# Performance work log

Measured on AMD Instinct MI355X. Metric: run time of the kernel, lower is better.

The kernel has to match this reference:

```python
import jax, jax.numpy as jnp
import numpy as np

B, S, H, D = 8, 16, 32, 64
HID = H * D
PAST = 4096


def setup_inputs() -> dict:
    key = jax.random.key(0)
    ks = jax.random.split(key, 7)
    sc = 0.02
    return {
        "hidden_states": jax.random.normal(ks[0], (B, S, HID), jnp.float32),
        "past_k": jax.random.normal(ks[1], (B, H, PAST, D), jnp.float32),
        "past_v": jax.random.normal(ks[2], (B, H, PAST, D), jnp.float32),
        "wq": jax.random.normal(ks[3], (HID, HID), jnp.float32) * sc,
        "wk": jax.random.normal(ks[4], (HID, HID), jnp.float32) * sc,
        "wv": jax.random.normal(ks[5], (HID, HID), jnp.float32) * sc,
        "wo": jax.random.normal(ks[6], (HID, HID), jnp.float32) * sc,
    }


def reference(hidden_states, past_k, past_v, wq, wk, wv, wo):
    b, s, _ = hidden_states.shape
    # QKV projections (torch Linear: x @ W.T), split into heads -> [B,H,S,D]
    q = (hidden_states @ wq.T).reshape(b, s, H, D).transpose(0, 2, 1, 3)
    k = (hidden_states @ wk.T).reshape(b, s, H, D).transpose(0, 2, 1, 3)
    v = (hidden_states @ wv.T).reshape(b, s, H, D).transpose(0, 2, 1, 3)
    # KV-cache concat: [B,H,past+S,D]
    k = jnp.concatenate([past_k, k], axis=2)
    v = jnp.concatenate([past_v, v], axis=2)
    scale = 1.0 / jnp.sqrt(jnp.asarray(D, hidden_states.dtype))
    # scores [B,H,S,T]
    scores = jnp.einsum("bhsd,bhtd->bhst", q, k) * scale
    probs = jax.nn.softmax(scores, axis=-1)
    out = jnp.einsum("bhst,bhtd->bhsd", probs, v)
    out = out.transpose(0, 2, 1, 3).reshape(b, s, HID)
    return out @ wo.T
```

## Files before the change

### kernel.cpp

```cpp
#include <hip/hip_runtime.h>
#include <hip/hip_bf16.h>
#include <stdint.h>

#define HID 2048
#define NH  32
#define HD  64
#define NB  8
#define NS  16
#define PAST 4096

#define QSCALE 0.18033688011112042591f

typedef __attribute__((ext_vector_type(8))) short short8;
typedef __attribute__((ext_vector_type(4))) short short4v;
typedef __attribute__((ext_vector_type(4))) float f32x4;

#define MFMA(a, b, c) __builtin_amdgcn_mfma_f32_16x16x32_bf16((a), (b), (c), 0, 0, 0)

#define PART_STRIDE 1088
#define NSPLIT 4

static __device__ __forceinline__ short f2bf(float f) {
    __hip_bfloat16 h = __float2bfloat16(f);
    return *reinterpret_cast<short*>(&h);
}

static __device__ __forceinline__ short8 pack8(float4 a, float4 b) {
    short8 r;
    r[0] = f2bf(a.x); r[1] = f2bf(a.y); r[2] = f2bf(a.z); r[3] = f2bf(a.w);
    r[4] = f2bf(b.x); r[5] = f2bf(b.y); r[6] = f2bf(b.z); r[7] = f2bf(b.w);
    return r;
}

static __device__ __forceinline__ short8 pack8s(float4 a, float4 b, float s) {
    short8 r;
    r[0] = f2bf(a.x * s); r[1] = f2bf(a.y * s); r[2] = f2bf(a.z * s); r[3] = f2bf(a.w * s);
    r[4] = f2bf(b.x * s); r[5] = f2bf(b.y * s); r[6] = f2bf(b.z * s); r[7] = f2bf(b.w * s);
    return r;
}

__global__ __launch_bounds__(256) void cvt_kernel(const float* __restrict__ in,
                                                  short* __restrict__ out) {
    int i = (blockIdx.x * 256 + threadIdx.x) * 4;
    float4 v = *reinterpret_cast<const float4*>(in + i);
    short4v o;
    o[0] = f2bf(v.x); o[1] = f2bf(v.y); o[2] = f2bf(v.z); o[3] = f2bf(v.w);
    *reinterpret_cast<short4v*>(out + i) = o;
}

__global__ __launch_bounds__(128) void proj_kernel(
        const short* __restrict__ X,
        const float* __restrict__ W0, const float* __restrict__ W1,
        const float* __restrict__ W2,
        float* __restrict__ Y0, float* __restrict__ Y1, float* __restrict__ Y2) {
    int mat   = blockIdx.x >> 9;
    int rest  = blockIdx.x & 511;
    int strip = rest >> 2, ks = rest & 3;
    int nbase = strip * 16;
    int k0    = ks * 512;
    const float* W = (mat == 0) ? W0 : (mat == 1) ? W1 : W2;
    float*       Y = (mat == 0) ? Y0 : (mat == 1) ? Y1 : Y2;

    int lane = threadIdx.x & 63;
    int wave = threadIdx.x >> 6;
    int lr = lane & 15, g = lane >> 4;

    f32x4 acc0 = {0.f, 0.f, 0.f, 0.f};
    f32x4 acc1 = {0.f, 0.f, 0.f, 0.f};
    f32x4 acc2 = {0.f, 0.f, 0.f, 0.f};
    f32x4 acc3 = {0.f, 0.f, 0.f, 0.f};

    const short* xr = X + (size_t)(wave * 64 + lr) * HID + g * 8 + k0;
    const float* wr = W + (size_t)(nbase + lr) * HID + g * 8 + k0;

    #pragma unroll 4
    for (int kc = 0; kc < 512; kc += 32) {
        float4 w0 = *reinterpret_cast<const float4*>(wr + kc);
        float4 w1 = *reinterpret_cast<const float4*>(wr + kc + 4);
        short8 bb = pack8(w0, w1);
        short8 a0 = *reinterpret_cast<const short8*>(xr + kc);
        short8 a1 = *reinterpret_cast<const short8*>(xr + (size_t)16 * HID + kc);
        short8 a2 = *reinterpret_cast<const short8*>(xr + (size_t)32 * HID + kc);
        short8 a3 = *reinterpret_cast<const short8*>(xr + (size_t)48 * HID + kc);
        acc0 = MFMA(a0, bb, acc0);
        acc1 = MFMA(a1, bb, acc1);
        acc2 = MFMA(a2, bb, acc2);
        acc3 = MFMA(a3, bb, acc3);
    }
    #define STACC(accv, f) do { \
        atomicAdd(&Y[(size_t)(wave * 64 + (f) * 16 + (g << 2) + 0) * HID + nbase + lr], accv[0]); \
        atomicAdd(&Y[(size_t)(wave * 64 + (f) * 16 + (g << 2) + 1) * HID + nbase + lr], accv[1]); \
        atomicAdd(&Y[(size_t)(wave * 64 + (f) * 16 + (g << 2) + 2) * HID + nbase + lr], accv[2]); \
        atomicAdd(&Y[(size_t)(wave * 64 + (f) * 16 + (g << 2) + 3) * HID + nbase + lr], accv[3]); \
    } while (0)
    STACC(acc0, 0); STACC(acc1, 1); STACC(acc2, 2); STACC(acc3, 3);
    #undef STACC
}

__global__ __launch_bounds__(256, 4) void attn_kernel(
        const float* __restrict__ q,
        const float* __restrict__ knew, const float* __restrict__ vnew,
        const float* __restrict__ pastK, const float* __restrict__ pastV,
        float* __restrict__ parts) {
    int bid = blockIdx.x;
    int bh = bid >> 2, split = bid & 3;
    int b = bh >> 5, h = bh & 31;
    int wave = threadIdx.x >> 6, lane = threadIdx.x & 63;
    int lq = lane & 15, g = lane >> 4;

    const float* qp = q + (size_t)(b * NS + lq) * HID + h * HD + g * 8;
    short8 qf0, qf1;
    {
        float4 a0 = *reinterpret_cast<const float4*>(qp);
        float4 a1 = *reinterpret_cast<const float4*>(qp + 4);
        float4 a2 = *reinterpret_cast<const float4*>(qp + 32);
        float4 a3 = *reinterpret_cast<const float4*>(qp + 36);
        qf0 = pack8s(a0, a1, QSCALE);
        qf1 = pack8s(a2, a3, QSCALE);
    }

    f32x4 o0 = {0.f, 0.f, 0.f, 0.f};
    f32x4 o1 = {0.f, 0.f, 0.f, 0.f};
    f32x4 o2 = {0.f, 0.f, 0.f, 0.f};
    f32x4 o3 = {0.f, 0.f, 0.f, 0.f};
    float m = -__builtin_inff(), lsum = 0.0f;

    const float* kbase = pastK + (size_t)bh * PAST * HD + (size_t)(split * 1024 + wave * 256) * HD;
    const float* vbase = pastV + (size_t)bh * PAST * HD + (size_t)(split * 1024 + wave * 256) * HD;

    #define LOADV8(dst, vtp, kfo, dcol) do { \
        dst[0] = f2bf((vtp)[(size_t)((kfo) + (g << 2) + 0) * HD + (dcol)]); \
        dst[1] = f2bf((vtp)[(size_t)((kfo) + (g << 2) + 1) * HD + (dcol)]); \
        dst[2] = f2bf((vtp)[(size_t)((kfo) + (g << 2) + 2) * HD + (dcol)]); \
        dst[3] = f2bf((vtp)[(size_t)((kfo) + (g << 2) + 3) * HD + (dcol)]); \
        dst[4] = f2bf((vtp)[(size_t)((kfo) + 16 + (g << 2) + 0) * HD + (dcol)]); \
        dst[5] = f2bf((vtp)[(size_t)((kfo) + 16 + (g << 2) + 1) * HD + (dcol)]); \
        dst[6] = f2bf((vtp)[(size_t)((kfo) + 16 + (g << 2) + 2) * HD + (dcol)]); \
        dst[7] = f2bf((vtp)[(size_t)((kfo) + 16 + (g << 2) + 3) * HD + (dcol)]); \
    } while (0)

    #define QKSUB(scv, s2i) do { \
        const float* kr = kbase + (size_t)(pb + (s2i) * 16 + lq) * HD + (g << 3); \
        float4 ka = *reinterpret_cast<const float4*>(kr); \
        float4 kb2 = *reinterpret_cast<const float4*>(kr + 4); \
        float4 kc2 = *reinterpret_cast<const float4*>(kr + 32); \
        float4 kd2 = *reinterpret_cast<const float4*>(kr + 36); \
        short8 af0 = pack8(ka, kb2); \
        short8 af1 = pack8(kc2, kd2); \
        f32x4 sv = {0.f, 0.f, 0.f, 0.f}; \
        sv = MFMA(af0, qf0, sv); \
        sv = MFMA(af1, qf1, sv); \
        scv = sv; \
    } while (0)

    #define PEXP(dst, idx, sv, r) do { \
        float e = exp2f(sv[r] - mn); rsum += e; dst[idx] = f2bf(e); \
    } while (0)

    #pragma unroll 1
    for (int t = 0; t < 4; ++t) {
        int pb = t * 64;

        const float* vt = vbase + (size_t)pb * HD;
        short8 vf0, vf1, vf2, vf3, vf4, vf5, vf6, vf7;
        LOADV8(vf0, vt, 0,  lq);       LOADV8(vf1, vt, 32, lq);
        LOADV8(vf2, vt, 0,  16 + lq);  LOADV8(vf3, vt, 32, 16 + lq);
        LOADV8(vf4, vt, 0,  32 + lq);  LOADV8(vf5, vt, 32, 32 + lq);
        LOADV8(vf6, vt, 0,  48 + lq);  LOADV8(vf7, vt, 32, 48 + lq);

        f32x4 sc0, sc1, sc2, sc3;
        QKSUB(sc0, 0); QKSUB(sc1, 1); QKSUB(sc2, 2); QKSUB(sc3, 3);

        float tmax = fmaxf(
            fmaxf(fmaxf(fmaxf(sc0[0], sc0[1]), fmaxf(sc0[2], sc0[3])),
                  fmaxf(fmaxf(sc1[0], sc1[1]), fmaxf(sc1[2], sc1[3]))),
            fmaxf(fmaxf(fmaxf(sc2[0], sc2[1]), fmaxf(sc2[2], sc2[3])),
                  fmaxf(fmaxf(sc3[0], sc3[1]), fmaxf(sc3[2], sc3[3]))));
        tmax = fmaxf(tmax, __shfl_xor(tmax, 16));
        tmax = fmaxf(tmax, __shfl_xor(tmax, 32));
        float mn = fmaxf(m, tmax);
        float alpha = exp2f(m - mn);
        float rsum = 0.f;
        short8 pf0, pf1;
        PEXP(pf0, 0, sc0, 0); PEXP(pf0, 1, sc0, 1); PEXP(pf0, 2, sc0, 2); PEXP(pf0, 3, sc0, 3);
        PEXP(pf0, 4, sc1, 0); PEXP(pf0, 5, sc1, 1); PEXP(pf0, 6, sc1, 2); PEXP(pf0, 7, sc1, 3);
        PEXP(pf1, 0, sc2, 0); PEXP(pf1, 1, sc2, 1); PEXP(pf1, 2, sc2, 2); PEXP(pf1, 3, sc2, 3);
        PEXP(pf1, 4, sc3, 0); PEXP(pf1, 5, sc3, 1); PEXP(pf1, 6, sc3, 2); PEXP(pf1, 7, sc3, 3);
        rsum += __shfl_xor(rsum, 16);
        rsum += __shfl_xor(rsum, 32);
        lsum = lsum * alpha + rsum;
        m = mn;
        o0 *= alpha; o1 *= alpha; o2 *= alpha; o3 *= alpha;

        o0 = MFMA(vf0, pf0, o0); o0 = MFMA(vf1, pf1, o0);
        o1 = MFMA(vf2, pf0, o1); o1 = MFMA(vf3, pf1, o1);
        o2 = MFMA(vf4, pf0, o2); o2 = MFMA(vf5, pf1, o2);
        o3 = MFMA(vf6, pf0, o3); o3 = MFMA(vf7, pf1, o3);
    }

    if (split == 0 && wave == 0) {
        const float* kr = knew + (size_t)(b * NS + lq) * HID + h * HD + g * 8;
        float4 ka = *reinterpret_cast<const float4*>(kr);
        float4 kb2 = *reinterpret_cast<const float4*>(kr + 4);
        float4 kc2 = *reinterpret_cast<const float4*>(kr + 32);
        float4 kd2 = *reinterpret_cast<const float4*>(kr + 36);
        short8 af0 = pack8(ka, kb2);
        short8 af1 = pack8(kc2, kd2);
        f32x4 sv = {0.f, 0.f, 0.f, 0.f};
        sv = MFMA(af0, qf0, sv);
        sv = MFMA(af1, qf1, sv);

        float tmax = fmaxf(fmaxf(sv[0], sv[1]), fmaxf(sv[2], sv[3]));
        tmax = fmaxf(tmax, __shfl_xor(tmax, 16));
        tmax = fmaxf(tmax, __shfl_xor(tmax, 32));
        float mn = fmaxf(m, tmax);
        float alpha = exp2f(m - mn);
        float e0 = exp2f(sv[0] - mn);
        float e1 = exp2f(sv[1] - mn);
        float e2 = exp2f(sv[2] - mn);
        float e3 = exp2f(sv[3] - mn);
        float rsum = e0 + e1 + e2 + e3;
        rsum += __shfl_xor(rsum, 16);
        rsum += __shfl_xor(rsum, 32);
        lsum = lsum * alpha + rsum;
        m = mn;
        o0 *= alpha; o1 *= alpha; o2 *= alpha; o3 *= alpha;

        short8 pfT;
        pfT[0] = f2bf(e0); pfT[1] = f2bf(e1); pfT[2] = f2bf(e2); pfT[3] = f2bf(e3);
        pfT[4] = 0; pfT[5] = 0; pfT[6] = 0; pfT[7] = 0;

        const float* vt = vnew + (size_t)(b * NS) * HID + h * HD;
        #define LOADVT(dst, dcol) do { \
            dst[0] = f2bf(vt[(size_t)((g << 2) + 0) * HID + (dcol)]); \
            dst[1] = f2bf(vt[(size_t)((g << 2) + 1) * HID + (dcol)]); \
            dst[2] = f2bf(vt[(size_t)((g << 2) + 2) * HID + (dcol)]); \
            dst[3] = f2bf(vt[(size_t)((g << 2) + 3) * HID + (dcol)]); \
            dst[4] = 0; dst[5] = 0; dst[6] = 0; dst[7] = 0; \
        } while (0)
        short8 vv0, vv1, vv2, vv3;
        LOADVT(vv0, lq); LOADVT(vv1, 16 + lq); LOADVT(vv2, 32 + lq); LOADVT(vv3, 48 + lq);
        #undef LOADVT
        o0 = MFMA(vv0, pfT, o0);
        o1 = MFMA(vv1, pfT, o1);
        o2 = MFMA(vv2, pfT, o2);
        o3 = MFMA(vv3, pfT, o3);
    }

    __shared__ float s_o[4][16][64];
    __shared__ float s_m[4][16];
    __shared__ float s_l[4][16];
    #define STO(ov, dt) do { \
        s_o[wave][lq][(dt) * 16 + (g << 2) + 0] = ov[0]; \
        s_o[wave][lq][(dt) * 16 + (g << 2) + 1] = ov[1]; \
        s_o[wave][lq][(dt) * 16 + (g << 2) + 2] = ov[2]; \
        s_o[wave][lq][(dt) * 16 + (g << 2) + 3] = ov[3]; \
    } while (0)
    STO(o0, 0); STO(o1, 1); STO(o2, 2); STO(o3, 3);
    #undef STO
    if (g == 0) { s_m[wave][lq] = m; s_l[wave][lq] = lsum; }
    __syncthreads();

    if (wave == 0) {
        float M = fmaxf(fmaxf(s_m[0][lq], s_m[1][lq]), fmaxf(s_m[2][lq], s_m[3][lq]));
        float aw0 = exp2f(s_m[0][lq] - M);
        float aw1 = exp2f(s_m[1][lq] - M);
        float aw2 = exp2f(s_m[2][lq] - M);
        float aw3 = exp2f(s_m[3][lq] - M);
        float L = aw0 * s_l[0][lq] + aw1 * s_l[1][lq] + aw2 * s_l[2][lq] + aw3 * s_l[3][lq];
        float* pbase = parts + (size_t)bid * PART_STRIDE;
        if (g == 0) { pbase[lq] = M; pbase[16 + lq] = L; }
        for (int dd = 0; dd < 16; ++dd) {
            int di = g * 16 + dd;
            float v = aw0 * s_o[0][lq][di] + aw1 * s_o[1][lq][di] +
                      aw2 * s_o[2][lq][di] + aw3 * s_o[3][lq][di];
            pbase[32 + lq * 64 + di] = v;
        }
    }
}

__global__ __launch_bounds__(256) void merge_kernel(const float* __restrict__ parts,
                                                    short* __restrict__ attnb) {
    int bh = blockIdx.x;
    int tid = threadIdx.x;
    int qi = tid >> 4, ds = (tid & 15) * 4;
    const float* p0 = parts + (size_t)(bh * NSPLIT) * PART_STRIDE;
    const float* p1 = p0 + PART_STRIDE;
    const float* p2 = p1 + PART_STRIDE;
    const float* p3 = p2 + PART_STRIDE;
    float m0 = p0[qi], m1 = p1[qi], m2 = p2[qi], m3 = p3[qi];
    float M = fmaxf(fmaxf(m0, m1), fmaxf(m2, m3));
    float a0 = exp2f(m0 - M), a1 = exp2f(m1 - M), a2 = exp2f(m2 - M), a3 = exp2f(m3 - M);
    float inv = 1.0f / (a0 * p0[16 + qi] + a1 * p1[16 + qi] +
                        a2 * p2[16 + qi] + a3 * p3[16 + qi]);
    int b = bh >> 5, h = bh & 31;
    int base = 32 + qi * 64 + ds;
    float v0 = (a0 * p0[base + 0] + a1 * p1[base + 0] + a2 * p2[base + 0] + a3 * p3[base + 0]) * inv;
    float v1 = (a0 * p0[base + 1] + a1 * p1[base + 1] + a2 * p2[base + 1] + a3 * p3[base + 1]) * inv;
    float v2 = (a0 * p0[base + 2] + a1 * p1[base + 2] + a2 * p2[base + 2] + a3 * p3[base + 2]) * inv;
    float v3 = (a0 * p0[base + 3] + a1 * p1[base + 3] + a2 * p2[base + 3] + a3 * p3[base + 3]) * inv;
    short4v o;
    o[0] = f2bf(v0); o[1] = f2bf(v1); o[2] = f2bf(v2); o[3] = f2bf(v3);
    *reinterpret_cast<short4v*>(attnb + (size_t)(b * NS + qi) * HID + h * HD + ds) = o;
}

extern "C" void kernel_launch(void* const* d_in, const int* in_sizes, int n_in,
                              void* d_out, int out_size, void* d_ws, size_t ws_size,
                              hipStream_t stream) {
    const float* hs     = (const float*)d_in[0];
    const float* past_k = (const float*)d_in[1];
    const float* past_v = (const float*)d_in[2];
    const float* wq     = (const float*)d_in[3];
    const float* wk     = (const float*)d_in[4];
    const float* wv     = (const float*)d_in[5];
    const float* wo     = (const float*)d_in[6];
    float* out = (float*)d_out;

    float* qb = (float*)d_ws;
    float* kn = qb + 128 * 2048;
    float* vn = kn + 128 * 2048;
    short* hsb   = (short*)(vn + 128 * 2048);
    short* attnb = hsb + 128 * 2048;
    float* parts = (float*)(attnb + 128 * 2048);

    hipMemsetAsync(qb, 0, (size_t)3 * 128 * 2048 * sizeof(float), stream);
    hipMemsetAsync(out, 0, (size_t)128 * 2048 * sizeof(float), stream);

    cvt_kernel<<<256, 256, 0, stream>>>(hs, hsb);
    proj_kernel<<<1536, 128, 0, stream>>>(hsb, wq, wk, wv, qb, kn, vn);
    attn_kernel<<<256 * NSPLIT, 256, 0, stream>>>(qb, kn, vn, past_k, past_v, parts);
    merge_kernel<<<256, 256, 0, stream>>>(parts, attnb);
    proj_kernel<<<512, 128, 0, stream>>>(attnb, wo, wo, wo, out, out, out);
}
```

Measured before the change: 179.6 us.

## Stage V tiles through per-wave LDS with coalesced loads and hoisted K loads

Previously each lane gathered V elements with strided scalar global loads to form the transposed MFMA operand. Now each wave loads V rows with coalesced float4 loads, converts them to bf16 into a padded per-wave LDS slab, and reads the transposed fragments back from LDS. K loads for all four subtiles are hoisted before the MFMAs to increase memory-level parallelism. The LDS slab is reused for the final cross-wave reduction behind an extra barrier, which adds LDS traffic and register pressure in exchange for fewer uncoalesced global accesses.

```diff
diff --git a/kernel.cpp b/kernel.cpp
--- a/kernel.cpp
+++ b/kernel.cpp
@@ -19,6 +19,7 @@
 
 #define PART_STRIDE 1088
 #define NSPLIT 4
+#define VSLAB  8704
 
 static __device__ __forceinline__ short f2bf(float f) {
     __hip_bfloat16 h = __float2bfloat16(f);
@@ -29,6 +30,12 @@
     short8 r;
     r[0] = f2bf(a.x); r[1] = f2bf(a.y); r[2] = f2bf(a.z); r[3] = f2bf(a.w);
     r[4] = f2bf(b.x); r[5] = f2bf(b.y); r[6] = f2bf(b.z); r[7] = f2bf(b.w);
+    return r;
+}
+
+static __device__ __forceinline__ short4v pack4(float4 a) {
+    short4v r;
+    r[0] = f2bf(a.x); r[1] = f2bf(a.y); r[2] = f2bf(a.z); r[3] = f2bf(a.w);
     return r;
 }
 
@@ -102,11 +109,17 @@
         const float* __restrict__ knew, const float* __restrict__ vnew,
         const float* __restrict__ pastK, const float* __restrict__ pastV,
         float* __restrict__ parts) {
+    __shared__ __align__(16) unsigned char lds_raw[4 * VSLAB];
+    __shared__ float s_m[4][16];
+    __shared__ float s_l[4][16];
+
     int bid = blockIdx.x;
     int bh = bid >> 2, split = bid & 3;
     int b = bh >> 5, h = bh & 31;
     int wave = threadIdx.x >> 6, lane = threadIdx.x & 63;
     int lq = lane & 15, g = lane >> 4;
+
+    unsigned short* vsl = (unsigned short*)(lds_raw + wave * VSLAB);
 
     const float* qp = q + (size_t)(b * NS + lq) * HID + h * HD + g * 8;
     short8 qf0, qf1;
@@ -128,31 +141,37 @@
     const float* kbase = pastK + (size_t)bh * PAST * HD + (size_t)(split * 1024 + wave * 256) * HD;
     const float* vbase = pastV + (size_t)bh * PAST * HD + (size_t)(split * 1024 + wave * 256) * HD;
 
-    #define LOADV8(dst, vtp, kfo, dcol) do { \
-        dst[0] = f2bf((vtp)[(size_t)((kfo) + (g << 2) + 0) * HD + (dcol)]); \
-        dst[1] = f2bf((vtp)[(size_t)((kfo) + (g << 2) + 1) * HD + (dcol)]); \
-        dst[2] = f2bf((vtp)[(size_t)((kfo) + (g << 2) + 2) * HD + (dcol)]); \
-        dst[3] = f2bf((vtp)[(size_t)((kfo) + (g << 2) + 3) * HD + (dcol)]); \
-        dst[4] = f2bf((vtp)[(size_t)((kfo) + 16 + (g << 2) + 0) * HD + (dcol)]); \
-        dst[5] = f2bf((vtp)[(size_t)((kfo) + 16 + (g << 2) + 1) * HD + (dcol)]); \
-        dst[6] = f2bf((vtp)[(size_t)((kfo) + 16 + (g << 2) + 2) * HD + (dcol)]); \
-        dst[7] = f2bf((vtp)[(size_t)((kfo) + 16 + (g << 2) + 3) * HD + (dcol)]); \
-    } while (0)
-
-    #define QKSUB(scv, s2i) do { \
-        const float* kr = kbase + (size_t)(pb + (s2i) * 16 + lq) * HD + (g << 3); \
-        float4 ka = *reinterpret_cast<const float4*>(kr); \
-        float4 kb2 = *reinterpret_cast<const float4*>(kr + 4); \
-        float4 kc2 = *reinterpret_cast<const float4*>(kr + 32); \
-        float4 kd2 = *reinterpret_cast<const float4*>(kr + 36); \
-        short8 af0 = pack8(ka, kb2); \
-        short8 af1 = pack8(kc2, kd2); \
+    #define KLD(s2i) \
+        const float* kr##s2i = kbase + (size_t)(pb + (s2i) * 16 + lq) * HD + (g << 3); \
+        float4 ka##s2i = *reinterpret_cast<const float4*>(kr##s2i); \
+        float4 kb##s2i = *reinterpret_cast<const float4*>(kr##s2i + 4); \
+        float4 kc##s2i = *reinterpret_cast<const float4*>(kr##s2i + 32); \
+        float4 kd##s2i = *reinterpret_cast<const float4*>(kr##s2i + 36);
+
+    #define KMM(scv, s2i) do { \
+        short8 af0 = pack8(ka##s2i, kb##s2i); \
+        short8 af1 = pack8(kc##s2i, kd##s2i); \
         f32x4 sv = {0.f, 0.f, 0.f, 0.f}; \
         sv = MFMA(af0, qf0, sv); \
         sv = MFMA(af1, qf1, sv); \
         scv = sv; \
     } while (0)
 
+    #define VLD(I) float4 vld##I = *reinterpret_cast<const float4*>(vt + (I) * 256 + lane * 4);
+    #define VST(I) *reinterpret_cast<short4v*>(vsl + (4 * (I) + g) * 68 + lq * 4) = pack4(vld##I);
+
+    #define LV(p, d) ((short)vsl[(p) * 68 + (d)])
+    #define VFR(dst, kfo, dcol) do { \
+        dst[0] = LV((kfo) + (g << 2) + 0, (dcol)); \
+        dst[1] = LV((kfo) + (g << 2) + 1, (dcol)); \
+        dst[2] = LV((kfo) + (g << 2) + 2, (dcol)); \
+        dst[3] = LV((kfo) + (g << 2) + 3, (dcol)); \
+        dst[4] = LV((kfo) + 16 + (g << 2) + 0, (dcol)); \
+        dst[5] = LV((kfo) + 16 + (g << 2) + 1, (dcol)); \
+        dst[6] = LV((kfo) + 16 + (g << 2) + 2, (dcol)); \
+        dst[7] = LV((kfo) + 16 + (g << 2) + 3, (dcol)); \
+    } while (0)
+
     #define PEXP(dst, idx, sv, r) do { \
         float e = exp2f(sv[r] - mn); rsum += e; dst[idx] = f2bf(e); \
     } while (0)
@@ -160,16 +179,15 @@
     #pragma unroll 1
     for (int t = 0; t < 4; ++t) {
         int pb = t * 64;
-
         const float* vt = vbase + (size_t)pb * HD;
-        short8 vf0, vf1, vf2, vf3, vf4, vf5, vf6, vf7;
-        LOADV8(vf0, vt, 0,  lq);       LOADV8(vf1, vt, 32, lq);
-        LOADV8(vf2, vt, 0,  16 + lq);  LOADV8(vf3, vt, 32, 16 + lq);
-        LOADV8(vf4, vt, 0,  32 + lq);  LOADV8(vf5, vt, 32, 32 + lq);
-        LOADV8(vf6, vt, 0,  48 + lq);  LOADV8(vf7, vt, 32, 48 + lq);
+
+        KLD(0) KLD(1) KLD(2) KLD(3)
+        VLD(0) VLD(1) VLD(2) VLD(3) VLD(4) VLD(5) VLD(6) VLD(7)
 
         f32x4 sc0, sc1, sc2, sc3;
-        QKSUB(sc0, 0); QKSUB(sc1, 1); QKSUB(sc2, 2); QKSUB(sc3, 3);
+        KMM(sc0, 0); KMM(sc1, 1); KMM(sc2, 2); KMM(sc3, 3);
+
+        VLD(8) VLD(9) VLD(10) VLD(11) VLD(12) VLD(13) VLD(14) VLD(15)
 
         float tmax = fmaxf(
             fmaxf(fmaxf(fmaxf(sc0[0], sc0[1]), fmaxf(sc0[2], sc0[3])),
@@ -192,10 +210,25 @@
         m = mn;
         o0 *= alpha; o1 *= alpha; o2 *= alpha; o3 *= alpha;
 
-        o0 = MFMA(vf0, pf0, o0); o0 = MFMA(vf1, pf1, o0);
-        o1 = MFMA(vf2, pf0, o1); o1 = MFMA(vf3, pf1, o1);
-        o2 = MFMA(vf4, pf0, o2); o2 = MFMA(vf5, pf1, o2);
-        o3 = MFMA(vf6, pf0, o3); o3 = MFMA(vf7, pf1, o3);
+        VST(0); VST(1); VST(2); VST(3); VST(4); VST(5); VST(6); VST(7);
+
+        {
+            short8 vfa;
+            VFR(vfa, 0, lq);       o0 = MFMA(vfa, pf0, o0);
+            VFR(vfa, 0, 16 + lq);  o1 = MFMA(vfa, pf0, o1);
+            VFR(vfa, 0, 32 + lq);  o2 = MFMA(vfa, pf0, o2);
+            VFR(vfa, 0, 48 + lq);  o3 = MFMA(vfa, pf0, o3);
+        }
+
+        VST(8); VST(9); VST(10); VST(11); VST(12); VST(13); VST(14); VST(15);
+
+        {
+            short8 vfb;
+            VFR(vfb, 32, lq);       o0 = MFMA(vfb, pf1, o0);
+            VFR(vfb, 32, 16 + lq);  o1 = MFMA(vfb, pf1, o1);
+            VFR(vfb, 32, 32 + lq);  o2 = MFMA(vfb, pf1, o2);
+            VFR(vfb, 32, 48 + lq);  o3 = MFMA(vfb, pf1, o3);
+        }
     }
 
     if (split == 0 && wave == 0) {
@@ -230,12 +263,12 @@
         pfT[0] = f2bf(e0); pfT[1] = f2bf(e1); pfT[2] = f2bf(e2); pfT[3] = f2bf(e3);
         pfT[4] = 0; pfT[5] = 0; pfT[6] = 0; pfT[7] = 0;
 
-        const float* vt = vnew + (size_t)(b * NS) * HID + h * HD;
+        const float* vt2 = vnew + (size_t)(b * NS) * HID + h * HD;
         #define LOADVT(dst, dcol) do { \
-            dst[0] = f2bf(vt[(size_t)((g << 2) + 0) * HID + (dcol)]); \
-            dst[1] = f2bf(vt[(size_t)((g << 2) + 1) * HID + (dcol)]); \
-            dst[2] = f2bf(vt[(size_t)((g << 2) + 2) * HID + (dcol)]); \
-            dst[3] = f2bf(vt[(size_t)((g << 2) + 3) * HID + (dcol)]); \
+            dst[0] = f2bf(vt2[(size_t)((g << 2) + 0) * HID + (dcol)]); \
+            dst[1] = f2bf(vt2[(size_t)((g << 2) + 1) * HID + (dcol)]); \
+            dst[2] = f2bf(vt2[(size_t)((g << 2) + 2) * HID + (dcol)]); \
+            dst[3] = f2bf(vt2[(size_t)((g << 2) + 3) * HID + (dcol)]); \
             dst[4] = 0; dst[5] = 0; dst[6] = 0; dst[7] = 0; \
         } while (0)
         short8 vv0, vv1, vv2, vv3;
@@ -247,14 +280,13 @@
         o3 = MFMA(vv3, pfT, o3);
     }
 
-    __shared__ float s_o[4][16][64];
-    __shared__ float s_m[4][16];
-    __shared__ float s_l[4][16];
+    __syncthreads();
+    float* so_w = (float*)(lds_raw + wave * VSLAB);
     #define STO(ov, dt) do { \
-        s_o[wave][lq][(dt) * 16 + (g << 2) + 0] = ov[0]; \
-        s_o[wave][lq][(dt) * 16 + (g << 2) + 1] = ov[1]; \
-        s_o[wave][lq][(dt) * 16 + (g << 2) + 2] = ov[2]; \
-        s_o[wave][lq][(dt) * 16 + (g << 2) + 3] = ov[3]; \
+        so_w[lq * 64 + (dt) * 16 + (g << 2) + 0] = ov[0]; \
+        so_w[lq * 64 + (dt) * 16 + (g << 2) + 1] = ov[1]; \
+        so_w[lq * 64 + (dt) * 16 + (g << 2) + 2] = ov[2]; \
+        so_w[lq * 64 + (dt) * 16 + (g << 2) + 3] = ov[3]; \
     } while (0)
     STO(o0, 0); STO(o1, 1); STO(o2, 2); STO(o3, 3);
     #undef STO
@@ -268,12 +300,16 @@
         float aw2 = exp2f(s_m[2][lq] - M);
         float aw3 = exp2f(s_m[3][lq] - M);
         float L = aw0 * s_l[0][lq] + aw1 * s_l[1][lq] + aw2 * s_l[2][lq] + aw3 * s_l[3][lq];
+        const float* so0 = (const float*)(lds_raw + 0 * VSLAB);
+        const float* so1 = (const float*)(lds_raw + 1 * VSLAB);
+        const float* so2 = (const float*)(lds_raw + 2 * VSLAB);
+        const float* so3 = (const float*)(lds_raw + 3 * VSLAB);
         float* pbase = parts + (size_t)bid * PART_STRIDE;
         if (g == 0) { pbase[lq] = M; pbase[16 + lq] = L; }
         for (int dd = 0; dd < 16; ++dd) {
             int di = g * 16 + dd;
-            float v = aw0 * s_o[0][lq][di] + aw1 * s_o[1][lq][di] +
-                      aw2 * s_o[2][lq][di] + aw3 * s_o[3][lq][di];
+            float v = aw0 * so0[lq * 64 + di] + aw1 * so1[lq * 64 + di] +
+                      aw2 * so2[lq * 64 + di] + aw3 * so3[lq * 64 + di];
             pbase[32 + lq * 64 + di] = v;
         }
     }
```

New measurement: 210.2 us. +17.0%, slower.
